# Kernel tuning notes

Hardware: AMD Instinct MI355X
Metric: run time of the kernel (lower is better)

## Reference

```python
import jax, jax.numpy as jnp
import numpy as np

B = 16
NS = [2048, 1024, 512, 256]
K = 12
GROUPS = 64
OUT = 1024
EPS = 1e-5


def setup_inputs() -> dict:
    key = jax.random.key(0)
    ks = iter(jax.random.split(key, 40))
    d = {}
    for i, n in enumerate(NS):
        d[f"fs{i}"] = jax.random.normal(next(ks), (B, n, 256), jnp.float32)
        d[f"xs{i}"] = jax.random.normal(next(ks), (B, n, 3), jnp.float32)
        ct = 1024 if i == 0 else 256
        d[f"ft{i}"] = jax.random.normal(next(ks), (B, n, ct), jnp.float32)
        d[f"xt{i}"] = jax.random.normal(next(ks), (B, n, 3), jnp.float32)
    d["Ws"] = jax.random.normal(next(ks), (4, OUT, 256), jnp.float32) * 0.05
    d["bWs"] = jax.random.normal(next(ks), (4, OUT), jnp.float32) * 0.05
    d["gs"] = jax.random.uniform(next(ks), (4, OUT), jnp.float32, 0.5, 1.5)
    d["bes"] = jax.random.normal(next(ks), (4, OUT), jnp.float32) * 0.05
    d["mus"] = jax.random.normal(next(ks), (4, OUT), jnp.float32) * 0.05
    d["vs"] = jax.random.uniform(next(ks), (4, OUT), jnp.float32, 0.5, 1.5)
    d["Wt0"] = jax.random.normal(next(ks), (OUT, 1024), jnp.float32) * 0.02
    d["Wt123"] = jax.random.normal(next(ks), (3, OUT, 256), jnp.float32) * 0.05
    d["bWt"] = jax.random.normal(next(ks), (4, OUT), jnp.float32) * 0.05
    d["gt"] = jax.random.uniform(next(ks), (4, OUT), jnp.float32, 0.5, 1.5)
    d["bet"] = jax.random.normal(next(ks), (4, OUT), jnp.float32) * 0.05
    d["mut"] = jax.random.normal(next(ks), (4, OUT), jnp.float32) * 0.05
    d["vt"] = jax.random.uniform(next(ks), (4, OUT), jnp.float32, 0.5, 1.5)
    return d


def fps(xyz, m):
    # furthest point sampling starting from index 0 (as in pointnet2_utils)
    b, n, _ = xyz.shape
    idxs = jnp.zeros((b, m), jnp.int32)
    d2 = jnp.full((b, n), 1e10, xyz.dtype)
    last = jnp.zeros((b,), jnp.int32)

    def body(i, st):
        idxs, d2, last = st
        lx = jnp.take_along_axis(xyz, last[:, None, None], axis=1)  # [b,1,3]
        d = jnp.sum((xyz - lx) ** 2, axis=-1)  # [b,n]
        d2 = jnp.minimum(d2, d)
        nxt = jnp.argmax(d2, axis=-1).astype(jnp.int32)
        return idxs.at[:, i].set(nxt), d2, nxt

    idxs, _, _ = jax.lax.fori_loop(1, m, body, (idxs, d2, last))
    return idxs


def gather_points(feat, idx):
    # feat [b,n,c], idx [b,...] -> [b,...,c]
    flat = idx.reshape(idx.shape[0], -1)
    out = jnp.take_along_axis(feat, flat[..., None], axis=1)
    return out.reshape(idx.shape + (feat.shape[-1],))


def knn_point(k, xyz, query):
    # squared pairwise distances [b,m,n]; k smallest (== torch.topk largest=False)
    d = (jnp.sum(query ** 2, -1, keepdims=True)
         - 2.0 * jnp.einsum('bmd,bnd->bmn', query, xyz)
         + jnp.sum(xyz ** 2, -1)[:, None, :])
    _, idx = jax.lax.top_k(-d, k)
    return idx.astype(jnp.int32)


def graph_op(grouped, w, b, g, be, mu, v):
    # grouped [B,M,K,C]; kernel-1 Conv1d == channel matmul; eval-mode BN; ReLU; max over K
    x = jnp.einsum('bmkc,oc->bmko', grouped, w) + b
    x = (x - mu) * (g * jax.lax.rsqrt(v + EPS)) + be
    x = jax.nn.relu(x)
    return jnp.max(x, axis=2)  # [B,M,O]


def reference(fs0, xs0, ft0, xt0, fs1, xs1, ft1, xt1, fs2, xs2, ft2, xt2,
              fs3, xs3, ft3, xt3, Ws, bWs, gs, bes, mus, vs,
              Wt0, Wt123, bWt, gt, bet, mut, vt):
    fs_list = [fs0, fs1, fs2, fs3]
    xs_list = [xs0, xs1, xs2, xs3]
    ft_list = [ft0, ft1, ft2, ft3]
    xt_list = [xt0, xt1, xt2, xt3]

    fps_idx = fps(xt_list[-1], GROUPS)              # [B,G]
    new_xyz = gather_points(xt_list[-1], fps_idx)   # [B,G,3]

    out_s, out_t = [], []
    for i in range(4):
        idx_t = knn_point(K, xt_list[i], new_xyz)   # [B,G,K]
        grp_t = gather_points(ft_list[i], idx_t)    # [B,G,K,Ct]
        idx_s = knn_point(K, xs_list[i], new_xyz)
        grp_s = gather_points(fs_list[i], idx_s)    # [B,G,K,256]
        wt = Wt0 if i == 0 else Wt123[i - 1]
        out_s.append(graph_op(grp_s, Ws[i], bWs[i], gs[i], bes[i], mus[i], vs[i]))
        out_t.append(graph_op(grp_t, wt, bWt[i], gt[i], bet[i], mut[i], vt[i]))
    return (tuple(out_s), tuple(out_t))
```

## Files before the change

### kernel.cpp

```cpp
#include <hip/hip_runtime.h>
#include <hip/hip_bf16.h>

#define DEVI __device__ __forceinline__

typedef __attribute__((ext_vector_type(8))) short bf16x8;
typedef __attribute__((ext_vector_type(16))) float f32x16;
typedef __attribute__((ext_vector_type(4))) unsigned int u32x4;
typedef __attribute__((ext_vector_type(4))) float fl4;

DEVI unsigned short f2bf(float f) {
  union { float f; unsigned u; } x; x.f = f;
  unsigned r = (x.u + 0x7fffu + ((x.u >> 16) & 1u)) >> 16;
  return (unsigned short)r;
}

DEVI unsigned cvtpk(float lo, float hi) {
  unsigned r;
  asm("v_cvt_pk_bf16_f32 %0, %1, %2" : "=v"(r) : "v"(lo), "v"(hi));
  return r;
}

DEVI float fadd3(float a, float b, float c) {
  return __fadd_rn(__fadd_rn(a, b), c);
}


__global__ __launch_bounds__(256) void prep2_kernel(
    const float* __restrict__ Ws, const float* __restrict__ Wt0,
    const float* __restrict__ Wt123,
    const float* __restrict__ bWs, const float* __restrict__ gs,
    const float* __restrict__ bes, const float* __restrict__ mus,
    const float* __restrict__ vs,
    const float* __restrict__ bWt, const float* __restrict__ gt,
    const float* __restrict__ bet, const float* __restrict__ mut,
    const float* __restrict__ vt, const float* __restrict__ xt3,
    char* __restrict__ wbf, float* __restrict__ bnA, float* __restrict__ bnB,
    float* __restrict__ newxyz) {
  const int blk = blockIdx.x;
  const int t = threadIdx.x;
  if (blk < 176) {
    int c, ntile, kt, NKT;
    if (blk < 64) { c = 4; NKT = 16; ntile = blk >> 4; kt = blk & 15; }
    else {
      int idx = blk - 64;
      int c7 = idx >> 4; c = (c7 < 4) ? c7 : c7 + 1;
      NKT = 4; ntile = (idx >> 2) & 3; kt = idx & 3;
    }
    const int o = ntile * 256 + t;
    const float* src;
    if (c < 4) src = Ws + (size_t)c * 262144 + o * 256 + kt * 64;
    else if (c == 4) src = Wt0 + (size_t)o * 1024 + kt * 64;
    else src = Wt123 + (size_t)(c - 5) * 262144 + o * 256 + kt * 64;
    const unsigned woffB[8] = {0u,       524288u,  1048576u, 1572864u,
                               2097152u, 4194304u, 4718592u, 5242880u};
    char* dst = wbf + woffB[c] + (size_t)(ntile * NKT + kt) * 32768u + t * 16;
#pragma unroll
    for (int s = 0; s < 8; ++s) {
      fl4 v0 = *reinterpret_cast<const fl4*>(src + s * 8);
      fl4 v1 = *reinterpret_cast<const fl4*>(src + s * 8 + 4);
      u32x4 w;
      w[0] = cvtpk(v0[0], v0[1]);
      w[1] = cvtpk(v0[2], v0[3]);
      w[2] = cvtpk(v1[0], v1[1]);
      w[3] = cvtpk(v1[2], v1[3]);
      *reinterpret_cast<u32x4*>(dst + s * 4096) = w;
    }
    return;
  }
  if (blk < 208) {
    unsigned r = (unsigned)(blk - 176) * 256u + t;
    unsigned c = r >> 10, o = r & 1023u;
    float g, bW, mu, v, be;
    if (c < 4u) { g = gs[r]; bW = bWs[r]; mu = mus[r]; v = vs[r]; be = bes[r]; }
    else {
      unsigned r2 = (c - 4u) * 1024u + o;
      g = gt[r2]; bW = bWt[r2]; mu = mut[r2]; v = vt[r2]; be = bet[r2];
    }
    float A = g / sqrtf(v + 1e-5f);
    float B = (bW - mu) * A + be;
    bnA[r] = A; bnB[r] = B;
    return;
  }
  const int b = blk - 208;
  if (t >= 64) return;
  const float* P = xt3 + (size_t)b * 256 * 3;
  float px[4], py[4], pz[4], d2[4];
#pragma unroll
  for (int j = 0; j < 4; ++j) {
    int p = t + 64 * j;
    px[j] = P[p * 3 + 0]; py[j] = P[p * 3 + 1]; pz[j] = P[p * 3 + 2];
    d2[j] = 1e10f;
  }
  float* NX = newxyz + (size_t)b * 64 * 3;
  float cx = __shfl(px[0], 0), cy = __shfl(py[0], 0), cz = __shfl(pz[0], 0);
  if (t == 0) { NX[0] = cx; NX[1] = cy; NX[2] = cz; }
  for (int i = 1; i < 64; ++i) {
    float bv = -1.0f; int bi = 0;
#pragma unroll
    for (int j = 0; j < 4; ++j) {
      float dx = __fsub_rn(px[j], cx), dy = __fsub_rn(py[j], cy),
            dz = __fsub_rn(pz[j], cz);
      float d = fadd3(__fmul_rn(dx, dx), __fmul_rn(dy, dy), __fmul_rn(dz, dz));
      d2[j] = fminf(d2[j], d);
      int p = t + 64 * j;
      if (j == 0) { bv = d2[0]; bi = t; }
      else if (d2[j] > bv) { bv = d2[j]; bi = p; }
    }
#pragma unroll
    for (int off = 32; off >= 1; off >>= 1) {
      float ov = __shfl_xor(bv, off);
      int oi = __shfl_xor(bi, off);
      if (ov > bv || (ov == bv && oi < bi)) { bv = ov; bi = oi; }
    }
    int s = bi;
    int owner = s & 63, slot = s >> 6;
    float sx = slot == 0 ? px[0] : slot == 1 ? px[1] : slot == 2 ? px[2] : px[3];
    float sy = slot == 0 ? py[0] : slot == 1 ? py[1] : slot == 2 ? py[2] : py[3];
    float sz = slot == 0 ? pz[0] : slot == 1 ? pz[1] : slot == 2 ? pz[2] : pz[3];
    cx = __shfl(sx, owner); cy = __shfl(sy, owner); cz = __shfl(sz, owner);
    if (t == 0) { NX[i * 3 + 0] = cx; NX[i * 3 + 1] = cy; NX[i * 3 + 2] = cz; }
  }
}

template <int NJ>
DEVI void knn_run(int lane, const float* __restrict__ X, float qx, float qy,
                  float qz, float qq, int* __restrict__ out) {
  float d2[NJ];
#pragma unroll
  for (int j = 0; j < NJ; ++j) {
    int pi = lane + 64 * j;
    float x = X[pi * 3 + 0], y = X[pi * 3 + 1], z = X[pi * 3 + 2];
    float xx = fadd3(__fmul_rn(x, x), __fmul_rn(y, y), __fmul_rn(z, z));
    float dot = fadd3(__fmul_rn(qx, x), __fmul_rn(qy, y), __fmul_rn(qz, z));
    d2[j] = __fadd_rn(__fsub_rn(qq, __fmul_rn(2.0f, dot)), xx);
  }
  for (int kk = 0; kk < 12; ++kk) {
    float bv = d2[0]; int bi = lane;
#pragma unroll
    for (int j = 1; j < NJ; ++j) {
      if (d2[j] < bv) { bv = d2[j]; bi = lane + 64 * j; }
    }
#pragma unroll
    for (int off = 1; off <= 32; off <<= 1) {
      float ov = __shfl_xor(bv, off);
      int oi = __shfl_xor(bi, off);
      if (ov < bv || (ov == bv && oi < bi)) { bv = ov; bi = oi; }
    }
    if (lane == 0) out[kk] = bi;
#pragma unroll
    for (int j = 0; j < NJ; ++j)
      if (bi == lane + 64 * j) d2[j] = 3.4e38f;
  }
}

struct KGP {
  const float* feat[8];
  const float* xyz[8];
  unsigned goffB[8];
};

__global__ __launch_bounds__(256) void knn_gather2_kernel(
    KGP p, const float* __restrict__ newxyz, char* __restrict__ grouped) {
  const int blk = blockIdx.x;
  int c, q0;
  if (blk < 256) { c = 4; q0 = 4096 + blk * 4; }
  else {
    int idx = blk - 256;
    int c7 = idx >> 8; c = (c7 < 4) ? c7 : c7 + 1;
    q0 = c * 1024 + (idx & 255) * 4;
  }
  const int scale = c & 3;
  const int n = 2048 >> scale;
  const int b = (q0 >> 6) & 15;
  const int g0 = q0 & 63;
  const int wid = threadIdx.x >> 6, lane = threadIdx.x & 63;
  __shared__ int idxs[4][12];
  const float* X = p.xyz[c] + (size_t)b * n * 3;
  {
    const int g = g0 + wid;
    const float* qp = newxyz + ((size_t)b * 64 + g) * 3;
    float qx = qp[0], qy = qp[1], qz = qp[2];
    float qq = fadd3(__fmul_rn(qx, qx), __fmul_rn(qy, qy), __fmul_rn(qz, qz));
    switch (scale) {
      case 0: knn_run<32>(lane, X, qx, qy, qz, qq, idxs[wid]); break;
      case 1: knn_run<16>(lane, X, qx, qy, qz, qq, idxs[wid]); break;
      case 2: knn_run<8>(lane, X, qx, qy, qz, qq, idxs[wid]); break;
      default: knn_run<4>(lane, X, qx, qy, qz, qq, idxs[wid]); break;
    }
  }
  __syncthreads();

  const int r = threadIdx.x & 63;
  const int sgrp = threadIdx.x >> 6;
  const int gl = r >> 4, kslot = r & 15;
  if (kslot >= 12) return;
  const int K = (c == 4) ? 1024 : 256;
  const int NKT = K >> 6;
  const int mtile = b * 4 + (g0 >> 4);
  const int rowT = (g0 & 15) * 16 + r;
  const int pidx = idxs[gl][kslot];
  const float* rowp = p.feat[c] + ((size_t)b * n + pidx) * K;
  char* dstb = grouped + p.goffB[c] + (size_t)mtile * NKT * 32768u + rowT * 16;
  for (int kt = 0; kt < NKT; ++kt) {
    char* dkt = dstb + (size_t)kt * 32768u;
    const float* skt = rowp + kt * 64;
#pragma unroll
    for (int ss = 0; ss < 2; ++ss) {
      int s = sgrp * 2 + ss;
      fl4 v0 = *reinterpret_cast<const fl4*>(skt + s * 8);
      fl4 v1 = *reinterpret_cast<const fl4*>(skt + s * 8 + 4);
      u32x4 w;
      w[0] = cvtpk(v0[0], v0[1]);
      w[1] = cvtpk(v0[2], v0[3]);
      w[2] = cvtpk(v1[0], v1[1]);
      w[3] = cvtpk(v1[2], v1[3]);
      *reinterpret_cast<u32x4*>(dkt + s * 4096) = w;
    }
  }
}

struct GemmPR {
  unsigned goff[8]; unsigned woff[8]; unsigned outoff[8];
  unsigned bnoff[8]; int K[8];
};

#define GLOAD_LDS16(gsrc, ldsdst)                                              \
  __builtin_amdgcn_global_load_lds(                                            \
      (const __attribute__((address_space(1))) void*)(gsrc),                   \
      (__attribute__((address_space(3))) void*)(ldsdst), 16, 0, 0)

__global__ __launch_bounds__(1024, 4) void gemm_pers_kernel(
    const char* __restrict__ grouped, const char* __restrict__ wbf,
    const float* __restrict__ bnA, const float* __restrict__ bnB,
    float* __restrict__ out, GemmPR p) {
  extern __shared__ char smem[];
  const int bid = blockIdx.x;
  const int xcd = bid & 7, slot = bid >> 3;
  const int rem = (xcd << 5) | slot;
  const int mtile = rem >> 2, ntile = rem & 3;
  const int tid = threadIdx.x;
  const int lane = tid & 63, wid = tid >> 6;
  const int wr = wid >> 2, wc = wid & 3;

  const int aoff = (lane >> 5) * 4096 + (wr * 64 + (lane & 31)) * 16;
  const int boff = (lane >> 5) * 4096 + (wc * 64 + (lane & 31)) * 16;

  f32x16 acc[2][2];
#pragma unroll
  for (int j = 0; j < 2; ++j)
#pragma unroll
    for (int nn = 0; nn < 2; ++nn)
#pragma unroll
      for (int e = 0; e < 16; ++e) acc[j][nn][e] = 0.f;

  auto stageA = [&](int par, const char* src) {
    char* dst = smem + par * 65536;
#pragma unroll
    for (int it = 0; it < 2; ++it)
      GLOAD_LDS16(src + (it * 1024 + tid) * 16, dst + (it * 1024 + wid * 64) * 16);
  };
  auto stageB = [&](int par, const char* src) {
    char* dst = smem + par * 65536 + 32768;
#pragma unroll
    for (int it = 0; it < 2; ++it)
      GLOAD_LDS16(src + (it * 1024 + tid) * 16, dst + (it * 1024 + wid * 64) * 16);
  };

  int nkt = p.K[0] >> 6;
  const char* Ac = grouped + p.goff[0] + (size_t)mtile * nkt * 32768;
  const char* Bc = wbf + p.woff[0] + (size_t)ntile * nkt * 32768;

  stageA(0, Ac);
  stageB(0, Bc);
  __syncthreads();

  int gs = 0;
  for (int zi = 0; zi < 8; ++zi) {
    nkt = p.K[zi] >> 6;
    const char* An = nullptr;
    const char* Bn = nullptr;
    if (zi < 7) {
      int nktN = p.K[zi + 1] >> 6;
      An = grouped + p.goff[zi + 1] + (size_t)mtile * nktN * 32768;
      Bn = wbf + p.woff[zi + 1] + (size_t)ntile * nktN * 32768;
    }
    for (int kt = 0; kt < nkt; ++kt, ++gs) {
      const int par = gs & 1;
      const char* As = smem + par * 65536;
      const char* Bs = As + 32768;

      if (gs + 1 < 44) {
        int k1 = kt + 1;
        const char* sA, * sB;
        if (k1 < nkt) { sA = Ac + (size_t)k1 * 32768; sB = Bc + (size_t)k1 * 32768; }
        else { sA = An; sB = Bn; }
        stageA(par ^ 1, sA);
        stageB(par ^ 1, sB);
      }

      bf16x8 bv[4][2], af[4][2];
#pragma unroll
      for (int ks = 0; ks < 4; ++ks)
#pragma unroll
        for (int nn = 0; nn < 2; ++nn)
          bv[ks][nn] = *reinterpret_cast<const bf16x8*>(
              Bs + ks * 8192 + nn * 512 + boff);
#pragma unroll
      for (int ks = 0; ks < 4; ++ks)
#pragma unroll
        for (int j = 0; j < 2; ++j)
          af[ks][j] = *reinterpret_cast<const bf16x8*>(
              As + ks * 8192 + j * 512 + aoff);
#pragma unroll
      for (int ks = 0; ks < 4; ++ks)
#pragma unroll
        for (int j = 0; j < 2; ++j)
#pragma unroll
          for (int nn = 0; nn < 2; ++nn)
            acc[j][nn] = __builtin_amdgcn_mfma_f32_32x32x16_bf16(
                af[ks][j], bv[ks][nn], acc[j][nn], 0, 0, 0);

      __syncthreads();
    }

    const float* bA = bnA + p.bnoff[zi];
    const float* bB = bnB + p.bnoff[zi];
    float* O = out + (size_t)p.outoff[zi];
    const bool hi0 = (lane < 32);
#pragma unroll
    for (int nn = 0; nn < 2; ++nn) {
      int colb = ntile * 256 + wc * 64 + nn * 32 + (lane & 31);
      float sA = bA[colb], sB = bB[colb];
#pragma unroll
      for (int j = 0; j < 2; ++j) {
#pragma unroll
        for (int h = 0; h < 2; ++h) {
          float v = fmaxf(fmaxf(acc[j][nn][8 * h + 0], acc[j][nn][8 * h + 1]),
                          fmaxf(acc[j][nn][8 * h + 2], acc[j][nn][8 * h + 3]));
          float v2 = fmaxf(fmaxf(acc[j][nn][8 * h + 4], acc[j][nn][8 * h + 5]),
                           fmaxf(acc[j][nn][8 * h + 6], acc[j][nn][8 * h + 7]));
          if (hi0) v = fmaxf(v, v2);
          v = fmaxf(v, __shfl_xor(v, 32));
          if (hi0) {
            int grp = mtile * 16 + wr * 4 + j * 2 + h;
            float val = fmaf(v, sA, sB);
            O[(size_t)grp * 1024 + colb] = fmaxf(val, 0.f);
          }
        }
      }
    }
#pragma unroll
    for (int j = 0; j < 2; ++j)
#pragma unroll
      for (int nn = 0; nn < 2; ++nn)
#pragma unroll
        for (int e = 0; e < 16; ++e) acc[j][nn][e] = 0.f;
    Ac = An;
    Bc = Bn;
  }
}

extern "C" void kernel_launch(void* const* d_in, const int* in_sizes, int n_in,
                              void* d_out, int out_size, void* d_ws,
                              size_t ws_size, hipStream_t stream) {
  (void)in_sizes; (void)n_in; (void)out_size; (void)ws_size;
  const float *fs[4], *xs[4], *ft[4], *xt[4];
  for (int i = 0; i < 4; ++i) {
    fs[i] = (const float*)d_in[4 * i + 0];
    xs[i] = (const float*)d_in[4 * i + 1];
    ft[i] = (const float*)d_in[4 * i + 2];
    xt[i] = (const float*)d_in[4 * i + 3];
  }
  const float* Ws = (const float*)d_in[16];
  const float* bWs = (const float*)d_in[17];
  const float* gs = (const float*)d_in[18];
  const float* bes = (const float*)d_in[19];
  const float* mus = (const float*)d_in[20];
  const float* vs = (const float*)d_in[21];
  const float* Wt0 = (const float*)d_in[22];
  const float* Wt123 = (const float*)d_in[23];
  const float* bWt = (const float*)d_in[24];
  const float* gt = (const float*)d_in[25];
  const float* bet = (const float*)d_in[26];
  const float* mut = (const float*)d_in[27];
  const float* vt = (const float*)d_in[28];

  char* ws = (char*)d_ws;
  float* newxyz = (float*)(ws + 0);
  float* bnA = (float*)(ws + 409600);
  float* bnB = (float*)(ws + 442368);
  char* wbf = ws + 475136;
  char* grouped = ws + 6242304;

  const unsigned goffB[8] = {0u,        8388608u,  16777216u, 25165824u,
                             33554432u, 67108864u, 75497472u, 83886080u};
  const unsigned woffB[8] = {0u,       524288u,  1048576u, 1572864u,
                             2097152u, 4194304u, 4718592u, 5242880u};

  prep2_kernel<<<224, 256, 0, stream>>>(Ws, Wt0, Wt123, bWs, gs, bes, mus, vs,
                                        bWt, gt, bet, mut, vt, xt[3], wbf, bnA,
                                        bnB, newxyz);

  KGP kg;
  for (int c = 0; c < 8; ++c) {
    int scale = c & 3;
    kg.feat[c] = (c < 4) ? fs[scale] : ft[scale];
    kg.xyz[c] = (c < 4) ? xs[scale] : xt[scale];
    kg.goffB[c] = goffB[c];
  }
  knn_gather2_kernel<<<2048, 256, 0, stream>>>(kg, newxyz, grouped);

  static const int co[8] = {0, 1, 2, 3, 5, 6, 7, 4};
  GemmPR mp;
  for (int zi = 0; zi < 8; ++zi) {
    int c = co[zi];
    mp.goff[zi] = goffB[c]; mp.woff[zi] = woffB[c];
    mp.outoff[zi] = (unsigned)c * 1048576u;
    mp.bnoff[zi] = (unsigned)c * 1024u;
    mp.K[zi] = (c == 4) ? 1024 : 256;
  }
  (void)hipFuncSetAttribute((const void*)gemm_pers_kernel,
                            hipFuncAttributeMaxDynamicSharedMemorySize, 131072);
  gemm_pers_kernel<<<256, 1024, 131072, stream>>>(grouped, wbf, bnA, bnB,
                                                  (float*)d_out, mp);
}
```

Baseline: 199.5 us.

## Halve GEMM tile width and K-stage depth to double block count

The persistent GEMM now launches 512 blocks of 512 threads instead of 256 blocks of 1024. Each block covers half the N columns (128 instead of 256) and stages K in 32-wide slabs, so shared memory drops from 128KB to 48KB. The aim is to fill more CUs, possibly fitting more blocks per CU, and to shorten each pipeline stage. The cost is more A-tile reloads across N tiles and twice as many stage iterations and barriers.

```diff
diff --git a/kernel.cpp b/kernel.cpp
--- a/kernel.cpp
+++ b/kernel.cpp
@@ -229,21 +229,25 @@
       (const __attribute__((address_space(1))) void*)(gsrc),                   \
       (__attribute__((address_space(3))) void*)(ldsdst), 16, 0, 0)
 
-__global__ __launch_bounds__(1024, 4) void gemm_pers_kernel(
+__global__ __launch_bounds__(512, 4) void gemm_pers_kernel(
     const char* __restrict__ grouped, const char* __restrict__ wbf,
     const float* __restrict__ bnA, const float* __restrict__ bnB,
     float* __restrict__ out, GemmPR p) {
   extern __shared__ char smem[];
   const int bid = blockIdx.x;
   const int xcd = bid & 7, slot = bid >> 3;
-  const int rem = (xcd << 5) | slot;
-  const int mtile = rem >> 2, ntile = rem & 3;
+  const int rem = (xcd << 6) | slot;
+  const int mtile = rem >> 3;
+  const int nt2 = rem & 7;
   const int tid = threadIdx.x;
   const int lane = tid & 63, wid = tid >> 6;
-  const int wr = wid >> 2, wc = wid & 3;
+  const int wr = wid >> 1, wc = wid & 1;
 
   const int aoff = (lane >> 5) * 4096 + (wr * 64 + (lane & 31)) * 16;
-  const int boff = (lane >> 5) * 4096 + (wc * 64 + (lane & 31)) * 16;
+  const int boff = (lane >> 5) * 2048 + (wc * 64 + (lane & 31)) * 16;
+  const int bS = wid >> 1;
+  const int bRow = (nt2 & 1) * 128 + (wid & 1) * 64 + lane;
+  const int bSrcOff = bS * 4096 + bRow * 16;
 
   f32x16 acc[2][2];
 #pragma unroll
@@ -253,22 +257,21 @@
 #pragma unroll
       for (int e = 0; e < 16; ++e) acc[j][nn][e] = 0.f;
 
-  auto stageA = [&](int par, const char* src) {
-    char* dst = smem + par * 65536;
+  auto stageA = [&](int par, const char* srcSlab) {
+    char* dst = smem + par * 16384;
 #pragma unroll
     for (int it = 0; it < 2; ++it)
-      GLOAD_LDS16(src + (it * 1024 + tid) * 16, dst + (it * 1024 + wid * 64) * 16);
+      GLOAD_LDS16(srcSlab + (it * 512 + tid) * 16,
+                  dst + (it * 512 + wid * 64) * 16);
   };
-  auto stageB = [&](int par, const char* src) {
-    char* dst = smem + par * 65536 + 32768;
-#pragma unroll
-    for (int it = 0; it < 2; ++it)
-      GLOAD_LDS16(src + (it * 1024 + tid) * 16, dst + (it * 1024 + wid * 64) * 16);
+  auto stageB = [&](int par, const char* srcSlab) {
+    char* dst = smem + 32768 + par * 8192 + wid * 1024;
+    GLOAD_LDS16(srcSlab + bSrcOff, dst);
   };
 
-  int nkt = p.K[0] >> 6;
-  const char* Ac = grouped + p.goff[0] + (size_t)mtile * nkt * 32768;
-  const char* Bc = wbf + p.woff[0] + (size_t)ntile * nkt * 32768;
+  int nst = (p.K[0] >> 6) * 2;
+  const char* Ac = grouped + p.goff[0] + (size_t)mtile * (nst >> 1) * 32768;
+  const char* Bc = wbf + p.woff[0] + (size_t)(nt2 >> 1) * (nst >> 1) * 32768;
 
   stageA(0, Ac);
   stageB(0, Bc);
@@ -276,43 +279,44 @@
 
   int gs = 0;
   for (int zi = 0; zi < 8; ++zi) {
-    nkt = p.K[zi] >> 6;
+    nst = (p.K[zi] >> 6) * 2;
     const char* An = nullptr;
     const char* Bn = nullptr;
     if (zi < 7) {
       int nktN = p.K[zi + 1] >> 6;
       An = grouped + p.goff[zi + 1] + (size_t)mtile * nktN * 32768;
-      Bn = wbf + p.woff[zi + 1] + (size_t)ntile * nktN * 32768;
-    }
-    for (int kt = 0; kt < nkt; ++kt, ++gs) {
+      Bn = wbf + p.woff[zi + 1] + (size_t)(nt2 >> 1) * nktN * 32768;
+    }
+    for (int st = 0; st < nst; ++st, ++gs) {
       const int par = gs & 1;
-      const char* As = smem + par * 65536;
-      const char* Bs = As + 32768;
-
-      if (gs + 1 < 44) {
-        int k1 = kt + 1;
-        const char* sA, * sB;
-        if (k1 < nkt) { sA = Ac + (size_t)k1 * 32768; sB = Bc + (size_t)k1 * 32768; }
-        else { sA = An; sB = Bn; }
-        stageA(par ^ 1, sA);
-        stageB(par ^ 1, sB);
+      const char* As = smem + par * 16384;
+      const char* Bs = smem + 32768 + par * 8192;
+
+      if (gs + 1 < 88) {
+        const char* nA;
+        const char* nB;
+        if (st + 1 < nst) {
+          nA = Ac + (size_t)(st + 1) * 16384;
+          nB = Bc + (size_t)(st + 1) * 16384;
+        } else { nA = An; nB = Bn; }
+        stageA(par ^ 1, nA);
+        stageB(par ^ 1, nB);
       }
 
-      bf16x8 bv[4][2], af[4][2];
-#pragma unroll
-      for (int ks = 0; ks < 4; ++ks)
-#pragma unroll
-        for (int nn = 0; nn < 2; ++nn)
-          bv[ks][nn] = *reinterpret_cast<const bf16x8*>(
-              Bs + ks * 8192 + nn * 512 + boff);
-#pragma unroll
-      for (int ks = 0; ks < 4; ++ks)
+      bf16x8 af[2][2], bv[2][2];
+#pragma unroll
+      for (int ks = 0; ks < 2; ++ks) {
 #pragma unroll
         for (int j = 0; j < 2; ++j)
           af[ks][j] = *reinterpret_cast<const bf16x8*>(
               As + ks * 8192 + j * 512 + aoff);
 #pragma unroll
-      for (int ks = 0; ks < 4; ++ks)
+        for (int nn = 0; nn < 2; ++nn)
+          bv[ks][nn] = *reinterpret_cast<const bf16x8*>(
+              Bs + ks * 4096 + nn * 512 + boff);
+      }
+#pragma unroll
+      for (int ks = 0; ks < 2; ++ks)
 #pragma unroll
         for (int j = 0; j < 2; ++j)
 #pragma unroll
@@ -329,7 +333,7 @@
     const bool hi0 = (lane < 32);
 #pragma unroll
     for (int nn = 0; nn < 2; ++nn) {
-      int colb = ntile * 256 + wc * 64 + nn * 32 + (lane & 31);
+      int colb = nt2 * 128 + wc * 64 + nn * 32 + (lane & 31);
       float sA = bA[colb], sB = bB[colb];
 #pragma unroll
       for (int j = 0; j < 2; ++j) {
@@ -420,7 +424,7 @@
     mp.K[zi] = (c == 4) ? 1024 : 256;
   }
   (void)hipFuncSetAttribute((const void*)gemm_pers_kernel,
-                            hipFuncAttributeMaxDynamicSharedMemorySize, 131072);
-  gemm_pers_kernel<<<256, 1024, 131072, stream>>>(grouped, wbf, bnA, bnB,
-                                                  (float*)d_out, mp);
-}
+                            hipFuncAttributeMaxDynamicSharedMemorySize, 49152);
+  gemm_pers_kernel<<<512, 512, 49152, stream>>>(grouped, wbf, bnA, bnB,
+                                                (float*)d_out, mp);
+}
```

After: 210.0 us. +5.3%, slower.
